# Kernel tuning notes

Measured on AMD Instinct MI355X. Metric: run time of the kernel, lower is better.

The kernel has to match this reference:

```python
import jax, jax.numpy as jnp
import numpy as np

N_NODES = 100000
N_EDGES = 3200000
N_FEAT = 128
EMBED = 20
N_CLASSES = 10
N_GRAPHS = 64


def setup_inputs() -> dict:
    key = jax.random.key(0)
    ks = jax.random.split(key, 8)
    x = jax.random.normal(ks[0], (N_NODES, N_FEAT), dtype=jnp.float32)
    edge_index = jax.random.randint(ks[1], (2, N_EDGES), 0, N_NODES, dtype=jnp.int64)
    edge_weights = jax.random.uniform(ks[2], (N_EDGES,), dtype=jnp.float32)
    batch = jnp.sort(jax.random.randint(ks[3], (N_NODES,), 0, N_GRAPHS, dtype=jnp.int64))
    # GCNConv parameters (glorot-ish scale) and final linear layer
    W = jax.random.normal(ks[4], (N_FEAT, EMBED), dtype=jnp.float32) * (1.0 / np.sqrt(N_FEAT))
    b = jnp.zeros((EMBED,), dtype=jnp.float32)
    lin_W = jax.random.normal(ks[5], (2 * EMBED, N_CLASSES), dtype=jnp.float32) * (1.0 / np.sqrt(2 * EMBED))
    lin_b = jnp.zeros((N_CLASSES,), dtype=jnp.float32)
    return {"x": x, "edge_index": edge_index, "edge_weights": edge_weights,
            "batch": batch, "W": W, "b": b, "lin_W": lin_W, "lin_b": lin_b}


def reference(x, edge_index, edge_weights, batch, W, b, lin_W, lin_b):
    N = x.shape[0]
    # --- GCNConv with self-loops and symmetric normalization (PyG semantics) ---
    loops = jnp.arange(N, dtype=edge_index.dtype)
    src = jnp.concatenate([edge_index[0], loops])
    dst = jnp.concatenate([edge_index[1], loops])
    w = jnp.concatenate([edge_weights, jnp.ones((N,), dtype=edge_weights.dtype)])
    deg = jax.ops.segment_sum(w, dst, num_segments=N)  # degree at targets
    dinv = jnp.where(deg > 0, jax.lax.rsqrt(deg), 0.0)
    norm = dinv[src] * w * dinv[dst]  # [E+N]
    xw = x @ W  # [N, EMBED]
    msg = xw[src] * norm[:, None]  # gather + scale
    out1 = jax.ops.segment_sum(msg, dst, num_segments=N) + b  # scatter-add
    # --- L2 normalize per node (F.normalize p=2 dim=1, eps=1e-12), then ReLU ---
    nrm = jnp.sqrt(jnp.sum(out1 * out1, axis=1, keepdims=True))
    embed = jax.nn.relu(out1 / jnp.maximum(nrm, 1e-12))
    # --- global max / mean pool per graph ---
    mx = jax.ops.segment_max(embed, batch, num_segments=N_GRAPHS)
    mx = jnp.where(jnp.isfinite(mx), mx, 0.0)  # empty graphs -> 0
    cnt = jax.ops.segment_sum(jnp.ones((N,), dtype=embed.dtype), batch, num_segments=N_GRAPHS)
    mean = jax.ops.segment_sum(embed, batch, num_segments=N_GRAPHS) / jnp.maximum(cnt, 1.0)[:, None]
    pooled = jnp.concatenate([mx, mean], axis=-1)  # [G, 2*EMBED]
    return pooled @ lin_W + lin_b
```

## Files before the change

kernel.cpp:

```cpp
#include <hip/hip_runtime.h>
#include <hip/hip_fp16.h>

#define NN 100000
#define NE 3200000
#define NF 128
#define EM 20
#define NC 10
#define NG 64

#define NB 782
#define CAPB 4608
#define T 4096
#define SBLK 1024

__global__ __launch_bounds__(SBLK) void k_scatter(
        const int* __restrict__ src, const int* __restrict__ dst,
        const float* __restrict__ w, int* __restrict__ gcursor,
        uint2* __restrict__ barr) {
    __shared__ unsigned int cnt[1024];
    __shared__ unsigned int off[1024];
    __shared__ unsigned int gbase[NB];
    __shared__ unsigned int wsum[16];
    __shared__ uint2 staged[T];
    __shared__ unsigned short bkt[T];
    int tid = threadIdx.x;
    long E0 = (long)blockIdx.x * T;
    int tot = (int)min((long)T, (long)NE - E0);
    cnt[tid] = 0;
    __syncthreads();
    unsigned int dreg[T / SBLK];
#pragma unroll
    for (int k = 0; k < T / SBLK; ++k) {
        int e = k * SBLK + tid;
        dreg[k] = 0;
        if (e < tot) {
            dreg[k] = (unsigned)dst[E0 + e];
            atomicAdd(&cnt[dreg[k] >> 7], 1u);
        }
    }
    __syncthreads();
    {
        int lane = tid & 63, wv = tid >> 6;
        unsigned int v = cnt[tid];
        unsigned int s = v;
#pragma unroll
        for (int o = 1; o < 64; o <<= 1) {
            unsigned int t = __shfl_up(s, o);
            if (lane >= o) s += t;
        }
        if (lane == 63) wsum[wv] = s;
        __syncthreads();
        if (tid == 0) {
            unsigned int a = 0;
#pragma unroll
            for (int i = 0; i < 16; ++i) { unsigned int t = wsum[i]; wsum[i] = a; a += t; }
        }
        __syncthreads();
        off[tid] = wsum[wv] + s - v;
    }
    __syncthreads();
    if (tid < NB) {
        unsigned int c = cnt[tid];
        gbase[tid] = c ? (unsigned int)atomicAdd(&gcursor[tid], (int)c) : 0u;
        cnt[tid] = 0;
    }
    __syncthreads();
#pragma unroll
    for (int k = 0; k < T / SBLK; ++k) {
        int e = k * SBLK + tid;
        if (e < tot) {
            long ge = E0 + e;
            unsigned int d = dreg[k];
            unsigned int b = d >> 7;
            unsigned int slot = atomicAdd(&cnt[b], 1u);
            unsigned int pos = off[b] + slot;
            staged[pos] = make_uint2((((unsigned)src[ge]) << 7) | (d & 127u),
                                     __float_as_uint(w[ge]));
            bkt[pos] = (unsigned short)b;
        }
    }
    __syncthreads();
    for (int i = tid; i < tot; i += SBLK) {
        unsigned int b = bkt[i];
        unsigned int gpos = gbase[b] + ((unsigned)i - off[b]);
        if (gpos < CAPB) barr[(size_t)b * CAPB + gpos] = staged[i];
    }
}

__global__ __launch_bounds__(512) void k_degxw(
        const int* __restrict__ gcursor, const uint2* __restrict__ barr,
        const float* __restrict__ x, const float* __restrict__ W,
        float* __restrict__ dinv,
        __half* __restrict__ xwhA, __half* __restrict__ xwhB) {
    __shared__ float xs[128 * 129];
    __shared__ float Ws[NF * EM];
    __shared__ float dacc[128];
    __shared__ float dvs[128];
    int bk = blockIdx.x, tid = threadIdx.x;
    if (tid < 128) dacc[tid] = 0.f;
    int base = bk * 128;
    const float4* xg = (const float4*)(x + (size_t)base * NF);
    size_t lim4 = (size_t)NN * NF / 4;
    size_t base4 = (size_t)base * NF / 4;
    float4 xv[8];
#pragma unroll
    for (int u = 0; u < 8; ++u) {
        int v = u * 512 + tid;
        xv[u] = (base4 + v < lim4) ? xg[v] : make_float4(0.f, 0.f, 0.f, 0.f);
    }
    for (int i = tid; i < NF * EM; i += 512) Ws[i] = W[i];
    __syncthreads();
    int cntb = min(gcursor[bk], CAPB);
    const uint2* row = barr + (size_t)bk * CAPB;
    for (int i = tid; i < cntb; i += 512) {
        uint2 r = row[i];
        atomicAdd(&dacc[r.x & 127u], __uint_as_float(r.y));
    }
#pragma unroll
    for (int u = 0; u < 8; ++u) {
        int v = u * 512 + tid;
        int fidx = v * 4;
        int r = fidx >> 7, c = fidx & 127;
        float* p = xs + r * 129 + c;
        p[0] = xv[u].x; p[1] = xv[u].y; p[2] = xv[u].z; p[3] = xv[u].w;
    }
    __syncthreads();
    if (tid < 128) {
        float dv = rsqrtf(1.0f + dacc[tid]);
        dvs[tid] = dv;
        int gd = base + tid;
        if (gd < NN) dinv[gd] = dv;
    }
    __syncthreads();
    int n = tid & 127;
    int jg = tid >> 7;
    int j0 = jg * 5;
    int node = base + n;
    if (node >= NN) return;
    float acc[5] = {0.f, 0.f, 0.f, 0.f, 0.f};
    const float* xr = xs + n * 129;
#pragma unroll 4
    for (int k = 0; k < NF; ++k) {
        float xvv = xr[k];
        const float* wr = Ws + k * EM + j0;
#pragma unroll
        for (int jj = 0; jj < 5; ++jj) acc[jj] = fmaf(xvv, wr[jj], acc[jj]);
    }
    float dv = dvs[n];
#pragma unroll
    for (int jj = 0; jj < 5; ++jj) {
        int j = j0 + jj;
        __half hv = __float2half(acc[jj] * dv);
        if (j < 16) xwhA[(size_t)node * 16 + j] = hv;
        else        xwhB[(size_t)node * 4 + (j - 16)] = hv;
    }
}

__device__ inline void unpack16(uint4 a0, uint4 a1, float* f) {
    const __half2* h = (const __half2*)&a0;
#pragma unroll
    for (int c = 0; c < 4; ++c) { float2 t = __half22float2(h[c]); f[2*c] = t.x; f[2*c+1] = t.y; }
    h = (const __half2*)&a1;
#pragma unroll
    for (int c = 0; c < 4; ++c) { float2 t = __half22float2(h[c]); f[8+2*c] = t.x; f[9+2*c] = t.y; }
}
__device__ inline void unpack4(uint2 b0, float* f) {
    const __half2* h = (const __half2*)&b0;
#pragma unroll
    for (int c = 0; c < 2; ++c) { float2 t = __half22float2(h[c]); f[2*c] = t.x; f[2*c+1] = t.y; }
}

__global__ void k_sortaggr(const int* __restrict__ gcursor,
                           const unsigned long long* __restrict__ barr64,
                           const __half* __restrict__ xwhA, const __half* __restrict__ xwhB,
                           const float* __restrict__ dinv, const float* __restrict__ b,
                           float* __restrict__ embed) {
    __shared__ unsigned long long srt[CAPB];
    __shared__ unsigned int cnt[128];
    __shared__ unsigned int off[128];
    __shared__ unsigned int wtot;
    int bk = blockIdx.x, tid = threadIdx.x;
    if (tid < 128) cnt[tid] = 0;
    __syncthreads();
    int cntb = min(gcursor[bk], CAPB);
    const unsigned long long* row = barr64 + (size_t)bk * CAPB;
    unsigned long long rec[9];
    unsigned int pos[9];
    int K = 0;
    for (int e = tid; e < cntb; e += 512) {
        rec[K] = row[e];
        pos[K] = atomicAdd(&cnt[(unsigned)rec[K] & 127u], 1u);
        ++K;
    }
    __syncthreads();
    unsigned int v = 0, s = 0;
    if (tid < 128) {
        v = cnt[tid]; s = v;
#pragma unroll
        for (int o = 1; o < 64; o <<= 1) {
            unsigned int t = __shfl_up(s, o);
            if ((tid & 63) >= o) s += t;
        }
        if (tid == 63) wtot = s;
    }
    __syncthreads();
    if (tid < 128) {
        if (tid >= 64) s += wtot;
        off[tid] = s;
    }
    __syncthreads();
    for (int k = 0; k < K; ++k) {
        unsigned int dl = (unsigned)rec[k] & 127u;
        srt[off[dl] - cnt[dl] + pos[k]] = rec[k];
    }
    __syncthreads();
    int d = tid >> 2, sub = tid & 3;
    int s0 = (int)(off[d] - cnt[d]), s1 = (int)off[d];
    const uint4* pA = (const uint4*)xwhA;
    const uint2* pB = (const uint2*)xwhB;
    float acc[20];
#pragma unroll
    for (int j = 0; j < 20; ++j) acc[j] = 0.f;
    for (int e = s0 + sub; e < s1; e += 4) {
        unsigned long long r = srt[e];
        unsigned int sN = ((unsigned int)r) >> 7;
        float nw = __uint_as_float((unsigned int)(r >> 32));
        uint4 a0 = pA[(size_t)sN * 2];
        uint4 a1 = pA[(size_t)sN * 2 + 1];
        uint2 b0 = pB[sN];
        float f[20];
        unpack16(a0, a1, f);
        unpack4(b0, f + 16);
#pragma unroll
        for (int j = 0; j < 20; ++j) acc[j] = fmaf(f[j], nw, acc[j]);
    }
#pragma unroll
    for (int j = 0; j < 20; ++j) {
        acc[j] += __shfl_xor(acc[j], 1);
        acc[j] += __shfl_xor(acc[j], 2);
    }
    if (sub == 0) {
        int gd = bk * 128 + d;
        if (gd < NN) {
            float dv = dinv[gd];
            uint4 a0 = pA[(size_t)gd * 2];
            uint4 a1 = pA[(size_t)gd * 2 + 1];
            uint2 b0 = pB[gd];
            float xdh[20];
            unpack16(a0, a1, xdh);
            unpack4(b0, xdh + 16);
            float r[20];
            float ss = 0.f;
#pragma unroll
            for (int j = 0; j < 20; ++j) {
                r[j] = dv * (acc[j] + xdh[j]) + b[j];
                ss = fmaf(r[j], r[j], ss);
            }
            float inv = 1.0f / fmaxf(sqrtf(ss), 1e-12f);
            float4 o4[5];
            float* o = (float*)o4;
#pragma unroll
            for (int j = 0; j < 20; ++j) {
                float e2 = r[j] * inv;
                o[j] = e2 > 0.f ? e2 : 0.f;
            }
            float4* eo = (float4*)(embed + (size_t)gd * EM);
#pragma unroll
            for (int c = 0; c < 5; ++c) eo[c] = o4[c];
        }
    }
}

__device__ inline int lbound(const int* __restrict__ batch, int key) {
    int lo = 0, hi = NN;
    while (lo < hi) {
        int mid = (lo + hi) >> 1;
        if (batch[mid] < key) lo = mid + 1; else hi = mid;
    }
    return lo;
}

__global__ void k_poolfinal(const float* __restrict__ embed, const int* __restrict__ batch,
                            const float* __restrict__ lw, const float* __restrict__ lb,
                            float* __restrict__ out) {
    __shared__ float cross[4][40];
    __shared__ float pooled[40];
    int g = blockIdx.x;
    int s0 = lbound(batch, g), s1 = lbound(batch, g + 1);
    int cnt = s1 - s0;
    float mx[EM], sm[EM];
#pragma unroll
    for (int j = 0; j < EM; ++j) { mx[j] = 0.f; sm[j] = 0.f; }
    for (int n = s0 + threadIdx.x; n < s1; n += 256) {
        const float4* e = (const float4*)(embed + (size_t)n * EM);
#pragma unroll
        for (int c = 0; c < 5; ++c) {
            float4 v = e[c];
            int j = c * 4;
            mx[j+0] = fmaxf(mx[j+0], v.x); sm[j+0] += v.x;
            mx[j+1] = fmaxf(mx[j+1], v.y); sm[j+1] += v.y;
            mx[j+2] = fmaxf(mx[j+2], v.z); sm[j+2] += v.z;
            mx[j+3] = fmaxf(mx[j+3], v.w); sm[j+3] += v.w;
        }
    }
#pragma unroll
    for (int o = 32; o > 0; o >>= 1) {
#pragma unroll
        for (int j = 0; j < EM; ++j) {
            mx[j] = fmaxf(mx[j], __shfl_xor(mx[j], o));
            sm[j] += __shfl_xor(sm[j], o);
        }
    }
    int wave = threadIdx.x >> 6, lane = threadIdx.x & 63;
    if (lane == 0) {
#pragma unroll
        for (int j = 0; j < EM; ++j) { cross[wave][j] = mx[j]; cross[wave][EM + j] = sm[j]; }
    }
    __syncthreads();
    if (threadIdx.x < 40) {
        int j = threadIdx.x;
        float v = cross[0][j];
        if (j < EM) v = fmaxf(fmaxf(v, cross[1][j]), fmaxf(cross[2][j], cross[3][j]));
        else        v = v + cross[1][j] + cross[2][j] + cross[3][j];
        if (j >= EM) v *= 1.0f / fmaxf((float)cnt, 1.0f);
        pooled[j] = v;
    }
    __syncthreads();
    if (threadIdx.x < NC) {
        int c = threadIdx.x;
        float acc = lb[c];
#pragma unroll
        for (int j = 0; j < 2 * EM; ++j) acc = fmaf(pooled[j], lw[j * NC + c], acc);
        out[g * NC + c] = acc;
    }
}

static inline size_t align_up(size_t v) { return (v + 1023) & ~(size_t)1023; }

extern "C" void kernel_launch(void* const* d_in, const int* in_sizes, int n_in,
                              void* d_out, int out_size, void* d_ws, size_t ws_size,
                              hipStream_t stream) {
    const float* x     = (const float*)d_in[0];
    const int*   ei    = (const int*)d_in[1];
    const float* ew    = (const float*)d_in[2];
    const int*   batch = (const int*)d_in[3];
    const float* W     = (const float*)d_in[4];
    const float* b     = (const float*)d_in[5];
    const float* lw    = (const float*)d_in[6];
    const float* lb    = (const float*)d_in[7];
    float* out = (float*)d_out;

    char* ws = (char*)d_ws;
    int*    gcursor = (int*)ws;    ws += align_up(4096);
    float*  dinv    = (float*)ws;  ws += align_up((size_t)NN * 4);
    __half* xwhA    = (__half*)ws; ws += align_up((size_t)NN * 16 * 2);
    __half* xwhB    = (__half*)ws; ws += align_up((size_t)NN * 4 * 2);
    float*  embed   = (float*)ws;  ws += align_up((size_t)NN * EM * 4);
    uint2*  barr    = (uint2*)ws;
    unsigned long long* barr64 = (unsigned long long*)barr;

    const int* srcp = ei;
    const int* dstp = ei + NE;

    (void)hipMemsetAsync(gcursor, 0, 4096, stream);
    k_scatter<<<(NE + T - 1) / T, SBLK, 0, stream>>>(srcp, dstp, ew, gcursor, barr);
    k_degxw<<<NB, 512, 0, stream>>>(gcursor, barr, x, W, dinv, xwhA, xwhB);
    k_sortaggr<<<NB, 512, 0, stream>>>(gcursor, barr64, xwhA, xwhB, dinv, b, embed);
    k_poolfinal<<<NG, 256, 0, stream>>>(embed, batch, lw, lb, out);
}
```

Before: 259.1 us.

## Read x rows directly from global in degxw, dropping the shared-memory staging tile

The k_degxw kernel no longer stages a 128x129 float tile of x in shared memory. Each thread now streams its node's row straight from global memory as float4 loads and does the matmul with W held in shared memory, overlapping that compute with the degree accumulation. Dropping about 66KB of LDS per block and adding launch_bounds min-blocks 8 aims to raise occupancy. The cost is poorly coalesced loads: each thread reads a separate 512-byte row, and the four thread groups read the same row again.

```diff
diff --git a/kernel.cpp b/kernel.cpp
--- a/kernel.cpp
+++ b/kernel.cpp
@@ -87,42 +87,47 @@
     }
 }
 
-__global__ __launch_bounds__(512) void k_degxw(
+__global__ __launch_bounds__(512, 8) void k_degxw(
         const int* __restrict__ gcursor, const uint2* __restrict__ barr,
         const float* __restrict__ x, const float* __restrict__ W,
         float* __restrict__ dinv,
         __half* __restrict__ xwhA, __half* __restrict__ xwhB) {
-    __shared__ float xs[128 * 129];
     __shared__ float Ws[NF * EM];
     __shared__ float dacc[128];
     __shared__ float dvs[128];
     int bk = blockIdx.x, tid = threadIdx.x;
     if (tid < 128) dacc[tid] = 0.f;
+    for (int i = tid; i < NF * EM; i += 512) Ws[i] = W[i];
+    __syncthreads();
     int base = bk * 128;
-    const float4* xg = (const float4*)(x + (size_t)base * NF);
-    size_t lim4 = (size_t)NN * NF / 4;
-    size_t base4 = (size_t)base * NF / 4;
-    float4 xv[8];
-#pragma unroll
-    for (int u = 0; u < 8; ++u) {
-        int v = u * 512 + tid;
-        xv[u] = (base4 + v < lim4) ? xg[v] : make_float4(0.f, 0.f, 0.f, 0.f);
-    }
-    for (int i = tid; i < NF * EM; i += 512) Ws[i] = W[i];
-    __syncthreads();
     int cntb = min(gcursor[bk], CAPB);
     const uint2* row = barr + (size_t)bk * CAPB;
     for (int i = tid; i < cntb; i += 512) {
         uint2 r = row[i];
         atomicAdd(&dacc[r.x & 127u], __uint_as_float(r.y));
     }
-#pragma unroll
-    for (int u = 0; u < 8; ++u) {
-        int v = u * 512 + tid;
-        int fidx = v * 4;
-        int r = fidx >> 7, c = fidx & 127;
-        float* p = xs + r * 129 + c;
-        p[0] = xv[u].x; p[1] = xv[u].y; p[2] = xv[u].z; p[3] = xv[u].w;
+    int n = tid & 127;
+    int jg = tid >> 7;
+    int j0 = jg * 5;
+    int node = base + n;
+    float acc[5] = {0.f, 0.f, 0.f, 0.f, 0.f};
+    if (node < NN) {
+        const float4* xr = (const float4*)(x + (size_t)node * NF);
+        for (int k4 = 0; k4 < NF / 4; ++k4) {
+            float4 xc = xr[k4];
+            const float* wr = Ws + (k4 * 4) * EM + j0;
+#pragma unroll
+            for (int jj = 0; jj < 5; ++jj) acc[jj] = fmaf(xc.x, wr[jj], acc[jj]);
+            wr += EM;
+#pragma unroll
+            for (int jj = 0; jj < 5; ++jj) acc[jj] = fmaf(xc.y, wr[jj], acc[jj]);
+            wr += EM;
+#pragma unroll
+            for (int jj = 0; jj < 5; ++jj) acc[jj] = fmaf(xc.z, wr[jj], acc[jj]);
+            wr += EM;
+#pragma unroll
+            for (int jj = 0; jj < 5; ++jj) acc[jj] = fmaf(xc.w, wr[jj], acc[jj]);
+        }
     }
     __syncthreads();
     if (tid < 128) {
@@ -132,27 +137,15 @@
         if (gd < NN) dinv[gd] = dv;
     }
     __syncthreads();
-    int n = tid & 127;
-    int jg = tid >> 7;
-    int j0 = jg * 5;
-    int node = base + n;
-    if (node >= NN) return;
-    float acc[5] = {0.f, 0.f, 0.f, 0.f, 0.f};
-    const float* xr = xs + n * 129;
-#pragma unroll 4
-    for (int k = 0; k < NF; ++k) {
-        float xvv = xr[k];
-        const float* wr = Ws + k * EM + j0;
-#pragma unroll
-        for (int jj = 0; jj < 5; ++jj) acc[jj] = fmaf(xvv, wr[jj], acc[jj]);
-    }
-    float dv = dvs[n];
-#pragma unroll
-    for (int jj = 0; jj < 5; ++jj) {
-        int j = j0 + jj;
-        __half hv = __float2half(acc[jj] * dv);
-        if (j < 16) xwhA[(size_t)node * 16 + j] = hv;
-        else        xwhB[(size_t)node * 4 + (j - 16)] = hv;
+    if (node < NN) {
+        float dv = dvs[n];
+#pragma unroll
+        for (int jj = 0; jj < 5; ++jj) {
+            int j = j0 + jj;
+            __half hv = __float2half(acc[jj] * dv);
+            if (j < 16) xwhA[(size_t)node * 16 + j] = hv;
+            else        xwhB[(size_t)node * 4 + (j - 16)] = hv;
+        }
     }
 }
 
```

New measurement: 262.8 us. Within noise of the previous version (+1.4%).
